# Performance work log

Hardware: AMD Instinct MI355X
Metric: run time of the kernel (lower is better)

The kernel has to match this reference:

```python
import jax, jax.numpy as jnp
import numpy as np
import itertools

B, T, C, H = 2, 512, 768, 12
HS = C // H                      # head size 64
M = 8                            # dpp_top_m
MIN_SIZE, MAX_SIZE = 2, 3        # subset sizes including token i
TEMP = 1.0                       # dpp_temperature
ALPHA = 1.0                      # dpp_penalty_alpha
SIGN = 1.0                       # minimize_det=False -> +log_det
NEG = -1e30

# Static combination tables over the M top-k candidate slots, lexicographic order.
# Filtering combos that touch i's slot (or padding slots) reproduces
# itertools.combinations(topidx_list) order exactly.
COMBS = [np.array(list(itertools.combinations(range(M), s)), dtype=np.int32)
         for s in range(MIN_SIZE - 1, MAX_SIZE)]  # extra sizes 1 and 2


def _token(i, q_i, k, v):
    Tn = k.shape[0]
    sim = k @ q_i                                   # [T]
    sim = jnp.where(jnp.arange(Tn) <= i, sim, -jnp.inf)  # causal
    _, top_idx = jax.lax.top_k(sim, M)              # [M]
    n_cand = jnp.minimum(M, i + 1)
    slot_valid = jnp.arange(M) < n_cand             # padding slots invalid
    slot_is_i = (top_idx == i) & slot_valid
    scores, outs, valids = [], [], []
    for comb in COMBS:
        slots = jnp.asarray(comb)                   # [nc, s]
        nc, s = comb.shape
        valid = slot_valid[slots].all(axis=1) & (~slot_is_i[slots].any(axis=1))
        idx = jnp.concatenate(
            [jnp.full((nc, 1), i, dtype=top_idx.dtype), top_idx[slots]], axis=1)  # [nc, s+1]
        K = k[idx]                                  # [nc, s+1, hs]
        V = v[idx]
        gram = jnp.einsum('cnd,cmd->cnm', K, K)     # [nc, s+1, s+1]
        det = jnp.linalg.det(gram)
        log_det = jnp.log(jnp.where(valid, det, 1.0) + 1e-6)
        score = SIGN * log_det / float(s + 1) ** ALPHA
        dot = jnp.einsum('cnd,d->cn', K, q_i) / HS ** 0.5
        w = jax.nn.softmax(dot, axis=1)
        out_s = jnp.einsum('cn,cnd->cd', w, V)      # [nc, hs]
        scores.append(jnp.where(valid, score, NEG))
        outs.append(out_s)
        valids.append(valid)
    scores = jnp.concatenate(scores)                # [36]
    outs = jnp.concatenate(outs, axis=0)            # [36, hs]
    has_valid = jnp.concatenate(valids).any()
    probs = jax.nn.softmax(scores / TEMP)
    best = jnp.argmax(probs)
    y_st = outs[best]
    y_soft = probs @ outs
    # straight-through: forward value = y_soft, gradient flows through y_st
    y = y_st + jax.lax.stop_gradient(y_soft - y_st)
    return jnp.where(has_valid, y, v[i])


def _dpp_head(q, k, v):  # q,k,v: [T, hs]
    return jax.vmap(lambda i, qi: _token(i, qi, k, v))(jnp.arange(q.shape[0]), q)


def _forward(x, W_attn, b_attn, W_proj, b_proj):
    Bx, Tx, Cx = x.shape
    qkv = x @ W_attn.T + b_attn                     # [B, T, 3C]
    q, k, v = jnp.split(qkv, 3, axis=2)

    def heads(t):  # [B, T, C] -> [B*H, T, hs]
        return t.reshape(Bx, Tx, H, HS).transpose(0, 2, 1, 3).reshape(Bx * H, Tx, HS)

    y = jax.vmap(_dpp_head)(heads(q), heads(k), heads(v))  # [B*H, T, hs]
    y = y.reshape(Bx, H, Tx, HS).transpose(0, 2, 1, 3).reshape(Bx, Tx, Cx)
    return y @ W_proj.T + b_proj


def setup_inputs() -> dict:
    key = jax.random.key(0)
    k1, k2, k3, k4, k5 = jax.random.split(key, 5)
    return {
        'x': jax.random.normal(k1, (B, T, C), dtype=jnp.float32),
        'W_attn': jax.random.normal(k2, (3 * C, C), dtype=jnp.float32) * 0.02,
        'b_attn': jax.random.normal(k3, (3 * C,), dtype=jnp.float32) * 0.02,
        'W_proj': jax.random.normal(k4, (C, C), dtype=jnp.float32) * 0.02,
        'b_proj': jax.random.normal(k5, (C,), dtype=jnp.float32) * 0.02,
    }


def reference(x, W_attn, b_attn, W_proj, b_proj):
    return _forward(x, W_attn, b_attn, W_proj, b_proj)
```

## Files before the change

### kernel.cpp

```cpp
#include <hip/hip_runtime.h>
#include <math.h>

#define Bn 2
#define Hn 12
#define Tn 512
#define Cn 768
#define HS 64
#define BH 24
#define MTOP 8
#define NCOMB 36
#define NEGV -1e30f

#define NX (Bn * Tn * Cn)
#define NW (3 * Cn * Cn)
#define NP (Cn * Cn)

typedef __bf16 bf16x8 __attribute__((ext_vector_type(8)));
typedef float f32x4 __attribute__((ext_vector_type(4)));

__device__ __constant__ int C_SL0[NCOMB] = {
  0,1,2,3,4,5,6,7,
  0,0,0,0,0,0,0,
  1,1,1,1,1,1,
  2,2,2,2,2,
  3,3,3,3,
  4,4,4,
  5,5,
  6};
__device__ __constant__ int C_SL1[NCOMB] = {
  -1,-1,-1,-1,-1,-1,-1,-1,
  1,2,3,4,5,6,7,
  2,3,4,5,6,7,
  3,4,5,6,7,
  4,5,6,7,
  5,6,7,
  6,7,
  7};

__device__ __constant__ int PA[45] = {
  0,0,0,0,0,0,0,0,0,
  1,1,1,1,1,1,1,1,
  2,2,2,2,2,2,2,
  3,3,3,3,3,3,
  4,4,4,4,4,
  5,5,5,5,
  6,6,6,
  7,7,
  8};
__device__ __constant__ int PB[45] = {
  0,1,2,3,4,5,6,7,8,
  1,2,3,4,5,6,7,8,
  2,3,4,5,6,7,8,
  3,4,5,6,7,8,
  4,5,6,7,8,
  5,6,7,8,
  6,7,8,
  7,8,
  8};

__device__ __constant__ int TI[36] = {
  0,1,1,2,2,2,3,3,3,3,4,4,4,4,4,5,5,5,5,5,5,6,6,6,6,6,6,6,7,7,7,7,7,7,7,7};
__device__ __constant__ int TJ[36] = {
  0,0,1,0,1,2,0,1,2,3,0,1,2,3,4,0,1,2,3,4,5,0,1,2,3,4,5,6,0,1,2,3,4,5,6,7};

__device__ __forceinline__ unsigned short bf_rne(float x) {
    unsigned u = __float_as_uint(x);
    return (unsigned short)((u + 0x7fff + ((u >> 16) & 1)) >> 16);
}
__device__ __forceinline__ float bf_f(unsigned short s) {
    return __uint_as_float(((unsigned)s) << 16);
}

template<int CTRL, int RM>
__device__ __forceinline__ float dpp_add_step(float x) {
    int t = __builtin_amdgcn_update_dpp(0, __float_as_int(x), CTRL, RM, 0xf, false);
    return x + __int_as_float(t);
}
template<int CTRL, int RM>
__device__ __forceinline__ float dpp_max_step(float x) {
    int t = __builtin_amdgcn_update_dpp((int)0xFF800000, __float_as_int(x), CTRL, RM, 0xf, false);
    return fmaxf(x, __int_as_float(t));
}
__device__ __forceinline__ float wave_sum(float x) {
    x = dpp_add_step<0x111, 0xf>(x);
    x = dpp_add_step<0x112, 0xf>(x);
    x = dpp_add_step<0x114, 0xf>(x);
    x = dpp_add_step<0x118, 0xf>(x);
    x = dpp_add_step<0x142, 0xa>(x);
    x = dpp_add_step<0x143, 0xc>(x);
    return __int_as_float(__builtin_amdgcn_readlane(__float_as_int(x), 63));
}
__device__ __forceinline__ float wave_max(float x) {
    x = dpp_max_step<0x111, 0xf>(x);
    x = dpp_max_step<0x112, 0xf>(x);
    x = dpp_max_step<0x114, 0xf>(x);
    x = dpp_max_step<0x118, 0xf>(x);
    x = dpp_max_step<0x142, 0xa>(x);
    x = dpp_max_step<0x143, 0xc>(x);
    return __int_as_float(__builtin_amdgcn_readlane(__float_as_int(x), 63));
}

__global__ __launch_bounds__(256) void conv_all(const float* __restrict__ x,
                                                const float* __restrict__ Wa,
                                                const float* __restrict__ Wp,
                                                unsigned short* __restrict__ xcat,
                                                unsigned short* __restrict__ Wcat,
                                                unsigned short* __restrict__ Wpbf) {
    int idx = blockIdx.x * 256 + threadIdx.x;
    if (idx < NX) {
        int r = idx / Cn, c = idx - r * Cn;
        float v = x[idx];
        unsigned short h = bf_rne(v);
        unsigned short l = bf_rne(v - bf_f(h));
        size_t base = (size_t)r * 2304 + c;
        xcat[base] = h;
        xcat[base + 768] = h;
        xcat[base + 1536] = l;
    } else if (idx < NX + NW) {
        int j = idx - NX;
        int r = j / Cn, c = j - r * Cn;
        float v = Wa[j];
        unsigned short h = bf_rne(v);
        unsigned short l = bf_rne(v - bf_f(h));
        size_t base = (size_t)r * 2304 + c;
        Wcat[base] = h;
        Wcat[base + 1536] = h;
        Wcat[base + 768] = l;
    } else if (idx < NX + NW + NP) {
        int j = idx - NX - NW;
        Wpbf[j] = bf_rne(Wp[j]);
    }
}

__device__ __forceinline__ void gld16(const unsigned short* g, unsigned short* l) {
    __builtin_amdgcn_global_load_lds(
        (const __attribute__((address_space(1))) unsigned short*)g,
        (__attribute__((address_space(3))) unsigned short*)l, 16, 0, 0);
}

__device__ __forceinline__ void gemm_core(const unsigned short* __restrict__ Ag,
                                          const unsigned short* __restrict__ Bg,
                                          int Kst, int NS,
                                          unsigned short* LB,
                                          f32x4 acc[2][2]) {
    const int tid = threadIdx.x;
    const int wv = tid >> 6, lane = tid & 63;
    const int r0 = tid >> 3;
    const int sg = tid & 7;
    const int gsg = sg ^ (r0 & 7);
    const int m0w = (wv >> 1) * 32;
    const int n0w = (wv & 1) * 32;
    const int fr = lane & 15;
    const int tq = lane >> 4;

    const unsigned short* pa0 = Ag + (size_t)r0 * Kst + gsg * 8;
    const unsigned short* pa1 = Ag + (size_t)(r0 + 32) * Kst + gsg * 8;
    const unsigned short* pb0 = Bg + (size_t)r0 * Kst + gsg * 8;
    const unsigned short* pb1 = Bg + (size_t)(r0 + 32) * Kst + gsg * 8;

    unsigned short* lA = LB + wv * 512;
    unsigned short* lB = LB + 4096 + wv * 512;

    auto issue = [&](int s, int b) {
        const int cb = s * 64;
        unsigned short* a  = lA + b * 8192;
        unsigned short* bb = lB + b * 8192;
        gld16(pa0 + cb, a);
        gld16(pa1 + cb, a + 2048);
        gld16(pb0 + cb, bb);
        gld16(pb1 + cb, bb + 2048);
    };

    auto compute = [&](int b) {
        const unsigned short* Ab = LB + b * 8192;
        const unsigned short* Bb = Ab + 4096;
        #pragma unroll
        for (int ks = 0; ks < 2; ++ks) {
            const int t = ks * 4 + tq;
            bf16x8 af[2], bg[2];
            #pragma unroll
            for (int mi = 0; mi < 2; ++mi) {
                const int row = m0w + 16 * mi + fr;
                af[mi] = *(const bf16x8*)(Ab + row * 64 + (t ^ (row & 7)) * 8);
            }
            #pragma unroll
            for (int ni = 0; ni < 2; ++ni) {
                const int row = n0w + 16 * ni + fr;
                bg[ni] = *(const bf16x8*)(Bb + row * 64 + (t ^ (row & 7)) * 8);
            }
            #pragma unroll
            for (int mi = 0; mi < 2; ++mi)
                #pragma unroll
                for (int ni = 0; ni < 2; ++ni)
                    acc[mi][ni] = __builtin_amdgcn_mfma_f32_16x16x32_bf16(af[mi], bg[ni], acc[mi][ni], 0, 0, 0);
        }
    };

    issue(0, 0);
    issue(1, 1);
    int b = 0;
    for (int s = 0; s < NS; ++s) {
        if (s + 1 < NS) asm volatile("s_waitcnt vmcnt(4)" ::: "memory");
        else            asm volatile("s_waitcnt vmcnt(0)" ::: "memory");
        __builtin_amdgcn_s_barrier();
        if (s + 2 < NS) {
            int bn = b + 2; if (bn >= 3) bn -= 3;
            issue(s + 2, bn);
        }
        compute(b);
        if (++b == 3) b = 0;
    }
}

__global__ __launch_bounds__(256) void mfma_qkv(const unsigned short* __restrict__ xcat,
                                                const unsigned short* __restrict__ Wcat,
                                                const float* __restrict__ bias,
                                                unsigned short* __restrict__ qcat,
                                                unsigned short* __restrict__ kcat,
                                                float* __restrict__ vh) {
    __shared__ __align__(16) unsigned short LB[3 * 8192];
    const int tm = blockIdx.x * 64;
    const int by = blockIdx.y;
    const int wv = threadIdx.x >> 6, lane = threadIdx.x & 63;
    const int kq = lane >> 4, r = lane & 15;
    f32x4 acc[2][2] = {};

    if (by < 24) {
        const int tn = by * 64;
        gemm_core(xcat + (size_t)tm * 2304, Wcat + (size_t)tn * 2304, 2304, 36, LB, acc);
        const int part = tn / Cn;
        #pragma unroll
        for (int mi = 0; mi < 2; ++mi) {
            #pragma unroll
            for (int ni = 0; ni < 2; ++ni) {
                #pragma unroll
                for (int rr = 0; rr < 4; ++rr) {
                    int mm = tm + (wv >> 1) * 32 + mi * 16 + kq * 4 + rr;
                    int nn = tn + (wv & 1) * 32 + ni * 16 + r;
                    float val = acc[mi][ni][rr] + bias[nn];
                    int bb = mm >> 9, t = mm & 511;
                    int c = nn - part * Cn;
                    int h = c >> 6, d = c & 63;
                    int bh = bb * Hn + h;
                    unsigned short s1 = bf_rne(val);
                    float r1 = val - bf_f(s1);
                    unsigned short s2 = bf_rne(r1);
                    unsigned short s3 = bf_rne(r1 - bf_f(s2));
                    size_t base = ((size_t)bh * Tn + t) * 384 + d;
                    if (part == 0) {
                        qcat[base]       = s1;
                        qcat[base + 64]  = s1;
                        qcat[base + 192] = s1;
                        qcat[base + 128] = s2;
                        qcat[base + 320] = s2;
                        qcat[base + 256] = s3;
                    } else {
                        kcat[base]       = s1;
                        kcat[base + 128] = s1;
                        kcat[base + 256] = s1;
                        kcat[base + 64]  = s2;
                        kcat[base + 320] = s2;
                        kcat[base + 192] = s3;
                    }
                }
            }
        }
    } else {
        const int hvi = by - 24;
        const int cv = hvi * 64;
        gemm_core(xcat + (size_t)tm * 2304,
                  Wcat + (size_t)(1536 + cv) * 2304, 2304, 12, LB, acc);
        #pragma unroll
        for (int mi = 0; mi < 2; ++mi) {
            #pragma unroll
            for (int ni = 0; ni < 2; ++ni) {
                #pragma unroll
                for (int rr = 0; rr < 4; ++rr) {
                    int mm = tm + (wv >> 1) * 32 + mi * 16 + kq * 4 + rr;
                    int nloc = (wv & 1) * 32 + ni * 16 + r;
                    float val = acc[mi][ni][rr] + bias[1536 + cv + nloc];
                    int bb = mm >> 9, t = mm & 511;
                    int bh = bb * Hn + hvi;
                    vh[((size_t)bh * Tn + t) * HS + nloc] = val;
                }
            }
        }
    }
}

__global__ __launch_bounds__(256) void mfma_sim(const unsigned short* __restrict__ qcat,
                                                const unsigned short* __restrict__ kcat,
                                                float* __restrict__ S) {
    __shared__ __align__(16) unsigned short LB[3 * 8192];
    const int bh = blockIdx.y;
    const int ti = TI[blockIdx.x], tj = TJ[blockIdx.x];
    f32x4 acc[2][2] = {};
    gemm_core(qcat + ((size_t)bh * Tn + ti * 64) * 384,
              kcat + ((size_t)bh * Tn + tj * 64) * 384, 384, 6, LB, acc);

    const int wv = threadIdx.x >> 6, lane = threadIdx.x & 63;
    const int kq = lane >> 4, r = lane & 15;
    float* Sp = S + (size_t)bh * 147456 + (size_t)(ti * (ti + 1) / 2 + tj) * 4096;
    #pragma unroll
    for (int mi = 0; mi < 2; ++mi)
        #pragma unroll
        for (int ni = 0; ni < 2; ++ni)
            #pragma unroll
            for (int rr = 0; rr < 4; ++rr) {
                int ml = (wv >> 1) * 32 + mi * 16 + kq * 4 + rr;
                int nl = (wv & 1) * 32 + ni * 16 + r;
                Sp[ml * 64 + nl] = acc[mi][ni][rr];
            }
}

__global__ __launch_bounds__(256) void mfma_proj(const unsigned short* __restrict__ Abf,
                                                 const unsigned short* __restrict__ Bbf,
                                                 const float* __restrict__ bias,
                                                 float* __restrict__ outp) {
    __shared__ __align__(16) unsigned short LB[3 * 8192];
    const int tm = blockIdx.x * 64;
    const int tn = blockIdx.y * 64;
    f32x4 acc[2][2] = {};
    gemm_core(Abf + (size_t)tm * Cn, Bbf + (size_t)tn * Cn, Cn, 12, LB, acc);

    const int wv = threadIdx.x >> 6, lane = threadIdx.x & 63;
    const int kq = lane >> 4, r = lane & 15;
    #pragma unroll
    for (int mi = 0; mi < 2; ++mi)
        #pragma unroll
        for (int ni = 0; ni < 2; ++ni)
            #pragma unroll
            for (int rr = 0; rr < 4; ++rr) {
                int mm = tm + (wv >> 1) * 32 + mi * 16 + kq * 4 + rr;
                int nn = tn + (wv & 1) * 32 + ni * 16 + r;
                outp[(size_t)mm * Cn + nn] = acc[mi][ni][rr] + bias[nn];
            }
}

#define CEF(arr, ia, ib) { \
    float _a = arr[ia], _b = arr[ib]; \
    arr[ia] = fmaxf(_a, _b); arr[ib] = fminf(_a, _b); }

__global__ __launch_bounds__(256, 8) void dpp_kernel(const float* __restrict__ S,
                                                     const unsigned short* __restrict__ kcat,
                                                     const float* __restrict__ vh,
                                                     unsigned short* __restrict__ yb) {
    const int bh = blockIdx.x;
    const int w = threadIdx.x >> 6;
    const int lane = threadIdx.x & 63;
    const int i = blockIdx.y * 4 + w;

    __shared__ float KshW[4][9][68];
    __shared__ float VshW[4][9][64];
    __shared__ float Gsh[4][81];
    __shared__ float qdsh[4][9];
    const float* Sbh = S + (size_t)bh * 147456;
    const unsigned short* kc = kcat + (size_t)bh * Tn * 384;
    const float* vbase = vh + (size_t)bh * Tn * HS;

    const int t8 = i >> 6;
    const int tribase = t8 * (t8 + 1) / 2;
    const int rloc = (i & 63) * 64;

    float sv[8];
    #pragma unroll
    for (int rr = 0; rr < 8; ++rr) {
        sv[rr] = -INFINITY;
        if (rr <= t8) {
            int j = rr * 64 + lane;
            float s = Sbh[(size_t)(tribase + rr) * 4096 + rloc + lane];
            sv[rr] = (j <= i) ? s : -INFINITY;
        }
    }
    const float qd0 = Sbh[(size_t)(tribase + t8) * 4096 + rloc + (i & 63)];

    float key[8];
    #pragma unroll
    for (int r = 0; r < 8; ++r) key[r] = sv[r];

    CEF(key,0,1) CEF(key,2,3) CEF(key,4,5) CEF(key,6,7)
    CEF(key,0,2) CEF(key,1,3) CEF(key,4,6) CEF(key,5,7)
    CEF(key,1,2) CEF(key,5,6)
    CEF(key,0,4) CEF(key,1,5) CEF(key,2,6) CEF(key,3,7)
    CEF(key,2,4) CEF(key,3,5)
    CEF(key,1,2) CEF(key,3,4) CEF(key,5,6)

    #pragma unroll
    for (int st = 0; st < 6; ++st) {
        const int off = 1 << st;
        float pk[8];
        #pragma unroll
        for (int r = 0; r < 8; ++r)
            pk[r] = __shfl_xor(key[r], off, 64);
        float t[8];
        #pragma unroll
        for (int r = 0; r < 8; ++r)
            t[r] = fmaxf(key[r], pk[7 - r]);
        CEF(t,0,4) CEF(t,1,5) CEF(t,2,6) CEF(t,3,7)
        CEF(t,0,2) CEF(t,1,3) CEF(t,4,6) CEF(t,5,7)
        CEF(t,0,1) CEF(t,2,3) CEF(t,4,5) CEF(t,6,7)
        #pragma unroll
        for (int r = 0; r < 8; ++r) key[r] = t[r];
    }

    int topi[8];
    {
        unsigned long long used[8] = {0, 0, 0, 0, 0, 0, 0, 0};
        #pragma unroll
        for (int p = 0; p < 8; ++p) {
            float v = key[p];
            int idx = i;
            bool found = false;
            #pragma unroll
            for (int r = 0; r < 8; ++r) {
                unsigned long long m = __ballot(sv[r] == v) & ~used[r];
                if (!found && m != 0ull) {
                    int l = __builtin_ctzll(m);
                    idx = r * 64 + l;
                    used[r] |= (1ull << l);
                    found = true;
                }
            }
            topi[p] = idx;
        }
    }

    #pragma unroll
    for (int a = 0; a < 9; ++a) {
        int t = (a == 0) ? i : topi[a - 1];
        size_t kb = (size_t)t * 384 + lane;
        KshW[w][a][lane] = bf_f(kc[kb]) + bf_f(kc[kb + 64]) + bf_f(kc[kb + 192]);
        VshW[w][a][lane] = vbase[(size_t)t * HS + lane];
    }
    if (lane < 9) {
        float val = qd0;
        #pragma unroll
        for (int p = 0; p < 8; ++p) if (lane == p + 1) val = key[p];
        qdsh[w][lane] = val;
    }

    if (lane < 45) {
        const int a = PA[lane], b = PB[lane];
        const float4* rka = (const float4*)&KshW[w][a][0];
        const float4* rkb = (const float4*)&KshW[w][b][0];
        float acc = 0.f;
        #pragma unroll
        for (int t = 0; t < 16; ++t) {
            float4 fa = rka[t], fb = rkb[t];
            acc += fa.x * fb.x; acc += fa.y * fb.y;
            acc += fa.z * fb.z; acc += fa.w * fb.w;
        }
        Gsh[w][a * 9 + b] = acc;
        Gsh[w][b * 9 + a] = acc;
    }

    const int sl0c = (lane < NCOMB) ? C_SL0[lane] : -1;
    const int sl1c = (lane < NCOMB) ? C_SL1[lane] : -1;
    float score = -INFINITY;
    int ca = 0, cb = 0, sdim = 1;
    {
        const int n_cand = (i + 1 < MTOP) ? (i + 1) : MTOP;
        int vmask = 0;
        #pragma unroll
        for (int s = 0; s < MTOP; ++s)
            if (s < n_cand && topi[s] != i) vmask |= (1 << s);

        if (lane < NCOMB) {
            sdim = (sl1c < 0) ? 1 : 2;
            ca = sl0c + 1;
            cb = (sl1c < 0) ? 0 : sl1c + 1;
            bool valid = ((vmask >> sl0c) & 1);
            if (sdim == 2) valid = valid && ((vmask >> sl1c) & 1);
            float G00 = Gsh[w][0];
            float Gaa = Gsh[w][ca * 9 + ca];
            float G0a = Gsh[w][ca];
            float det;
            if (sdim == 1) {
                det = G00 * Gaa - G0a * G0a;
            } else {
                float G0b = Gsh[w][cb];
                float Gab = Gsh[w][ca * 9 + cb];
                float Gbb = Gsh[w][cb * 9 + cb];
                det = G00 * (Gaa * Gbb - Gab * Gab)
                    - G0a * (G0a * Gbb - Gab * G0b)
                    + G0b * (G0a * Gab - Gaa * G0b);
            }
            score = valid ? (logf(det + 1e-6f) / (float)(sdim + 1)) : NEGV;
        }
    }

    const float mxv = wave_max(score);
    const float ee = (lane < NCOMB) ? expf(score - mxv) : 0.f;
    const float sumv = wave_sum(ee);

    float pwx = 0.f, pwy = 0.f, pwz = 0.f;
    if (lane < NCOMB) {
        float prob = ee / sumv;
        float d0 = qdsh[w][0]  * 0.125f;
        float d1 = qdsh[w][ca] * 0.125f;
        float d2 = (sdim == 2) ? qdsh[w][cb] * 0.125f : -INFINITY;
        float m2 = fmaxf(fmaxf(d0, d1), d2);
        float e0 = expf(d0 - m2), e1 = expf(d1 - m2);
        float e2 = (sdim == 2) ? expf(d2 - m2) : 0.f;
        float inv = prob / (e0 + e1 + e2);
        pwx = e0 * inv; pwy = e1 * inv; pwz = e2 * inv;
    }

    const float c0 = wave_sum(pwx);
    float cs[8];
    #pragma unroll
    for (int s = 0; s < 8; ++s) {
        float contrib = ((sl0c == s) ? pwy : 0.f) + ((sl1c == s) ? pwz : 0.f);
        cs[s] = wave_sum(contrib);
    }

    {
        const bool hasValid = (mxv > -1e29f);
        const float v0 = VshW[w][0][lane];
        float y = v0;
        if (hasValid) {
            y = c0 * v0;
            #pragma unroll
            for (int s = 0; s < 8; ++s)
                y += cs[s] * VshW[w][s + 1][lane];
        }
        const int bb = bh / Hn, h = bh % Hn;
        yb[((size_t)(bb * Tn + i)) * Cn + h * HS + lane] = bf_rne(y);
    }
}

extern "C" void kernel_launch(void* const* d_in, const int* in_sizes, int n_in,
                              void* d_out, int out_size, void* d_ws, size_t ws_size,
                              hipStream_t stream) {
    const float* x      = (const float*)d_in[0];
    const float* W_attn = (const float*)d_in[1];
    const float* b_attn = (const float*)d_in[2];
    const float* W_proj = (const float*)d_in[3];
    const float* b_proj = (const float*)d_in[4];
    float* out = (float*)d_out;

    char* ws = (char*)d_ws;
    float* vh            = (float*)(ws);
    unsigned short* qcat = (unsigned short*)(ws + 3145728);
    unsigned short* kcat = (unsigned short*)(ws + 12582912);
    unsigned short* xcat = (unsigned short*)(ws + 22020096);
    unsigned short* Wcat = (unsigned short*)(ws + 26738688);
    float* S             = (float*)(ws + 26738688);
    unsigned short* ybf  = xcat;
    unsigned short* Wpbf = (unsigned short*)(ws + 40894464);

    conv_all<<<dim3((NX + NW + NP + 255) / 256), 256, 0, stream>>>(
        x, W_attn, W_proj, xcat, Wcat, Wpbf);

    mfma_qkv<<<dim3(16, 36), 256, 0, stream>>>(xcat, Wcat, b_attn, qcat, kcat, vh);

    mfma_sim<<<dim3(36, BH), 256, 0, stream>>>(qcat, kcat, S);

    dpp_kernel<<<dim3(BH, Tn / 4), 256, 0, stream>>>(S, kcat, vh, ybf);

    mfma_proj<<<dim3(16, 12), 256, 0, stream>>>(ybf, Wpbf, b_proj, out);
}
```

Baseline: 136.0 us.

## Remap block indices for XCD-local L2 reuse and vectorize conversion kernel

All GEMM and DPP kernels switch to 1D grids whose block index is decoded so that blocks scheduled on the same XCD (blockIdx mod 8) work on the same head or output column group. The aim is better L2 cache reuse of shared operands such as Wcat slices and per-head K/S data. The conversion kernel also processes two elements per thread, using float2 loads and packed 32-bit stores. The index decoding assumes exact grid sizes and round-robin XCD dispatch, which holds only on this hardware.

```diff
diff --git a/kernel.cpp b/kernel.cpp
--- a/kernel.cpp
+++ b/kernel.cpp
@@ -106,29 +106,35 @@
                                                 unsigned short* __restrict__ xcat,
                                                 unsigned short* __restrict__ Wcat,
                                                 unsigned short* __restrict__ Wpbf) {
-    int idx = blockIdx.x * 256 + threadIdx.x;
+    const int idx = (blockIdx.x * 256 + threadIdx.x) * 2;
     if (idx < NX) {
         int r = idx / Cn, c = idx - r * Cn;
-        float v = x[idx];
-        unsigned short h = bf_rne(v);
-        unsigned short l = bf_rne(v - bf_f(h));
+        float2 v = *(const float2*)(x + idx);
+        unsigned short h0 = bf_rne(v.x), l0 = bf_rne(v.x - bf_f(h0));
+        unsigned short h1 = bf_rne(v.y), l1 = bf_rne(v.y - bf_f(h1));
+        unsigned ph = (unsigned)h0 | ((unsigned)h1 << 16);
+        unsigned pl = (unsigned)l0 | ((unsigned)l1 << 16);
         size_t base = (size_t)r * 2304 + c;
-        xcat[base] = h;
-        xcat[base + 768] = h;
-        xcat[base + 1536] = l;
+        *(unsigned*)(xcat + base)        = ph;
+        *(unsigned*)(xcat + base + 768)  = ph;
+        *(unsigned*)(xcat + base + 1536) = pl;
     } else if (idx < NX + NW) {
         int j = idx - NX;
         int r = j / Cn, c = j - r * Cn;
-        float v = Wa[j];
-        unsigned short h = bf_rne(v);
-        unsigned short l = bf_rne(v - bf_f(h));
+        float2 v = *(const float2*)(Wa + j);
+        unsigned short h0 = bf_rne(v.x), l0 = bf_rne(v.x - bf_f(h0));
+        unsigned short h1 = bf_rne(v.y), l1 = bf_rne(v.y - bf_f(h1));
+        unsigned ph = (unsigned)h0 | ((unsigned)h1 << 16);
+        unsigned pl = (unsigned)l0 | ((unsigned)l1 << 16);
         size_t base = (size_t)r * 2304 + c;
-        Wcat[base] = h;
-        Wcat[base + 1536] = h;
-        Wcat[base + 768] = l;
+        *(unsigned*)(Wcat + base)        = ph;
+        *(unsigned*)(Wcat + base + 1536) = ph;
+        *(unsigned*)(Wcat + base + 768)  = pl;
     } else if (idx < NX + NW + NP) {
         int j = idx - NX - NW;
-        Wpbf[j] = bf_rne(Wp[j]);
+        float2 v = *(const float2*)(Wp + j);
+        unsigned short h0 = bf_rne(v.x), h1 = bf_rne(v.y);
+        *(unsigned*)(Wpbf + j) = (unsigned)h0 | ((unsigned)h1 << 16);
     }
 }
 
@@ -219,8 +225,12 @@
                                                 unsigned short* __restrict__ kcat,
                                                 float* __restrict__ vh) {
     __shared__ __align__(16) unsigned short LB[3 * 8192];
-    const int tm = blockIdx.x * 64;
-    const int by = blockIdx.y;
+    const int xcd = blockIdx.x & 7;
+    const int v = blockIdx.x >> 3;
+    int tmi, by;
+    if (v < 48) { by = xcd * 3 + (v >> 4); tmi = v & 15; }
+    else        { int q = xcd * 24 + (v - 48); by = 24 + (q >> 4); tmi = q & 15; }
+    const int tm = tmi * 64;
     const int wv = threadIdx.x >> 6, lane = threadIdx.x & 63;
     const int kq = lane >> 4, r = lane & 15;
     f32x4 acc[2][2] = {};
@@ -292,8 +302,11 @@
                                                 const unsigned short* __restrict__ kcat,
                                                 float* __restrict__ S) {
     __shared__ __align__(16) unsigned short LB[3 * 8192];
-    const int bh = blockIdx.y;
-    const int ti = TI[blockIdx.x], tj = TJ[blockIdx.x];
+    const int xcd = blockIdx.x & 7;
+    const int v = blockIdx.x >> 3;
+    const int bh = xcd * 3 + v / 36;
+    const int tile = v % 36;
+    const int ti = TI[tile], tj = TJ[tile];
     f32x4 acc[2][2] = {};
     gemm_core(qcat + ((size_t)bh * Tn + ti * 64) * 384,
               kcat + ((size_t)bh * Tn + tj * 64) * 384, 384, 6, LB, acc);
@@ -318,8 +331,10 @@
                                                  const float* __restrict__ bias,
                                                  float* __restrict__ outp) {
     __shared__ __align__(16) unsigned short LB[3 * 8192];
-    const int tm = blockIdx.x * 64;
-    const int tn = blockIdx.y * 64;
+    const int xcd = blockIdx.x & 7;
+    const int q = xcd * 24 + (blockIdx.x >> 3);
+    const int tm = (q & 15) * 64;
+    const int tn = (q >> 4) * 64;
     f32x4 acc[2][2] = {};
     gemm_core(Abf + (size_t)tm * Cn, Bbf + (size_t)tn * Cn, Cn, 12, LB, acc);
 
@@ -345,10 +360,13 @@
                                                      const unsigned short* __restrict__ kcat,
                                                      const float* __restrict__ vh,
                                                      unsigned short* __restrict__ yb) {
-    const int bh = blockIdx.x;
+    const int xcd = blockIdx.x & 7;
+    const int vb = blockIdx.x >> 3;
+    const int bh = xcd * 3 + (vb >> 7);
+    const int iblk = vb & 127;
     const int w = threadIdx.x >> 6;
     const int lane = threadIdx.x & 63;
-    const int i = blockIdx.y * 4 + w;
+    const int i = iblk * 4 + w;
 
     __shared__ float KshW[4][9][68];
     __shared__ float VshW[4][9][64];
@@ -549,14 +567,14 @@
     unsigned short* ybf  = xcat;
     unsigned short* Wpbf = (unsigned short*)(ws + 40894464);
 
-    conv_all<<<dim3((NX + NW + NP + 255) / 256), 256, 0, stream>>>(
+    conv_all<<<dim3((NX + NW + NP) / 2 / 256), 256, 0, stream>>>(
         x, W_attn, W_proj, xcat, Wcat, Wpbf);
 
-    mfma_qkv<<<dim3(16, 36), 256, 0, stream>>>(xcat, Wcat, b_attn, qcat, kcat, vh);
-
-    mfma_sim<<<dim3(36, BH), 256, 0, stream>>>(qcat, kcat, S);
-
-    dpp_kernel<<<dim3(BH, Tn / 4), 256, 0, stream>>>(S, kcat, vh, ybf);
-
-    mfma_proj<<<dim3(16, 12), 256, 0, stream>>>(ybf, Wpbf, b_proj, out);
-}
+    mfma_qkv<<<dim3(576), 256, 0, stream>>>(xcat, Wcat, b_attn, qcat, kcat, vh);
+
+    mfma_sim<<<dim3(864), 256, 0, stream>>>(qcat, kcat, S);
+
+    dpp_kernel<<<dim3(3072), 256, 0, stream>>>(S, kcat, vh, ybf);
+
+    mfma_proj<<<dim3(192), 256, 0, stream>>>(ybf, Wpbf, b_proj, out);
+}
```

Result: faster. 128.8 us (-5.3%).
